# Kernel tuning notes

Hardware: AMD Instinct MI355X
Metric: run time of the kernel (lower is better)

The kernel has to match this reference:

```python
import jax, jax.numpy as jnp
import numpy as np
import math

B, S, H, D = 8, 4096, 768, 64  # batch, seq_len, hidden_dim, head_size


def setup_inputs() -> dict:
    key = jax.random.key(0)
    kx, kk, kq, kv, kbk, kbq, kbv = jax.random.split(key, 7)
    s = 1.0 / math.sqrt(H)
    return {
        "x": jax.random.normal(kx, (B, S, H), dtype=jnp.float32),
        "Wk": jax.random.normal(kk, (H, D), dtype=jnp.float32) * s,
        "bk": jax.random.normal(kbk, (D,), dtype=jnp.float32) * s,
        "Wq": jax.random.normal(kq, (H, D), dtype=jnp.float32) * s,
        "bq": jax.random.normal(kbq, (D,), dtype=jnp.float32) * s,
        "Wv": jax.random.normal(kv, (H, D), dtype=jnp.float32) * s,
        "bv": jax.random.normal(kbv, (D,), dtype=jnp.float32) * s,
    }


def reference(x, Wk, bk, Wq, bq, Wv, bv):
    # projections: [B, S, D]
    k = x @ Wk + bk
    q = x @ Wq + bq
    v = x @ Wv + bv
    # full O(S^2) attention scores, as in the original module
    weight = jnp.einsum("bqd,bkd->bqk", q, k)  # [B, S, S]
    causal = jnp.tril(jnp.ones((S, S), dtype=bool))
    # original masks first, then divides by sqrt(head_size); -inf/sqrt = -inf
    weight = jnp.where(causal, weight, -jnp.inf) / math.sqrt(D)
    weight = jax.nn.softmax(weight, axis=-1)
    # dropout p=0.0 (eval-mode reference): identity
    out = jnp.einsum("bqk,bkd->bqd", weight, v)  # [B, S, D]
    return out
```

## Files before the change

kernel.cpp:

```cpp
#include <hip/hip_runtime.h>
#include <hip/hip_bf16.h>
#include <math.h>

#define B_ 8
#define S_ 4096
#define H_ 768
#define D_ 64

typedef __bf16 bf16;
typedef bf16 bf16x8 __attribute__((ext_vector_type(8)));
typedef bf16 bf16x4 __attribute__((ext_vector_type(4)));
typedef float floatx4 __attribute__((ext_vector_type(4)));
typedef int  int4v  __attribute__((ext_vector_type(4)));

__device__ __forceinline__ int sw_off(int r, int chunk) {
    return r * 128 + ((chunk ^ (r & 7)) << 4);
}

__global__ __launch_bounds__(256) void wtrans_kernel(
    const float* __restrict__ Wq, const float* __restrict__ Wk,
    const float* __restrict__ Wv, bf16* __restrict__ wt)
{
    __shared__ bf16 t_lds[64][72];
    const float* W = (blockIdx.y == 0) ? Wq : (blockIdx.y == 1) ? Wk : Wv;
    bf16* o = wt + ((size_t)blockIdx.y * 12 + blockIdx.x) * 4096;
    const int k0 = blockIdx.x * 64;
    const int tid = threadIdx.x;
    #pragma unroll
    for (int rep = 0; rep < 16; ++rep) {
        int idx = rep * 256 + tid;
        int r = idx >> 6, n = idx & 63;
        t_lds[n][r] = (bf16)W[(size_t)(k0 + r) * D_ + n];
    }
    __syncthreads();
    #pragma unroll
    for (int rep = 0; rep < 16; ++rep) {
        int idx = rep * 256 + tid;
        int n = idx >> 6, kk = idx & 63;
        o[n * 64 + kk] = t_lds[n][kk];
    }
}

__global__ __launch_bounds__(256, 3) void proj_kernel(
    const float* __restrict__ x, const bf16* __restrict__ wt,
    const float* __restrict__ bq, const float* __restrict__ bk,
    const float* __restrict__ bv,
    bf16* __restrict__ qout, bf16* __restrict__ kout, bf16* __restrict__ vtt)
{
    __shared__ bf16 wlds[3][64 * 64];

    const int m0   = blockIdx.x * 64;
    const int tid  = threadIdx.x;
    const int lane = tid & 63;
    const int wave = tid >> 6;
    const int quad = lane >> 4;
    const int c    = lane & 15;
    const int mrow = m0 + wave * 16 + c;

    floatx4 acc[3][4] = {};
    const float* xrow = &x[(size_t)mrow * H_ + quad * 8];

    auto loadA = [&](int k0, bf16x8* dst) {
        #pragma unroll
        for (int s = 0; s < 2; ++s) {
            const float* xp = xrow + k0 + s * 32;
            float4 f0 = *(const float4*)xp;
            float4 f1 = *(const float4*)(xp + 4);
            bf16x8 a;
            a[0] = (bf16)f0.x; a[1] = (bf16)f0.y; a[2] = (bf16)f0.z; a[3] = (bf16)f0.w;
            a[4] = (bf16)f1.x; a[5] = (bf16)f1.y; a[6] = (bf16)f1.z; a[7] = (bf16)f1.w;
            dst[s] = a;
        }
    };
    auto loadW = [&](int kt, int4v g[3][2]) {
        #pragma unroll
        for (int w = 0; w < 3; ++w) {
            const char* s = (const char*)wt + (size_t)(w * 12 + kt) * 8192;
            g[w][0] = *(const int4v*)(s + tid * 16);
            g[w][1] = *(const int4v*)(s + tid * 16 + 4096);
        }
    };

    const int woff = sw_off(tid >> 3, tid & 7);

    bf16x8 afn[2]; loadA(0, afn);
    int4v g[3][2]; loadW(0, g);

    for (int kt = 0; kt < 12; ++kt) {
        __syncthreads();
        #pragma unroll
        for (int w = 0; w < 3; ++w) {
            *(int4v*)((char*)&wlds[w][0] + woff)        = g[w][0];
            *(int4v*)((char*)&wlds[w][0] + woff + 4096) = g[w][1];
        }
        bf16x8 af[2] = { afn[0], afn[1] };
        if (kt < 11) { loadW(kt + 1, g); loadA((kt + 1) * 64, afn); }
        __syncthreads();
        #pragma unroll
        for (int s = 0; s < 2; ++s) {
            #pragma unroll
            for (int w = 0; w < 3; ++w) {
                #pragma unroll
                for (int tn = 0; tn < 4; ++tn) {
                    const int r = tn * 16 + c;
                    bf16x8 bfrag = *(const bf16x8*)
                        ((const char*)&wlds[w][0] + sw_off(r, s * 4 + quad));
                    acc[w][tn] = __builtin_amdgcn_mfma_f32_16x16x32_bf16(
                        af[s], bfrag, acc[w][tn], 0, 0, 0);
                }
            }
        }
    }

    const int rbase = m0 + wave * 16 + quad * 4;
    #pragma unroll
    for (int tn = 0; tn < 4; ++tn) {
        const int n = tn * 16 + c;
        float bqv = bq[n];
        #pragma unroll
        for (int r = 0; r < 4; ++r)
            qout[(size_t)(rbase + r) * 128 + n] = (bf16)(acc[0][tn][r] + bqv);
        float bkv = bk[n];
        #pragma unroll
        for (int r = 0; r < 4; ++r)
            kout[(size_t)(rbase + r) * D_ + n] = (bf16)(acc[1][tn][r] + bkv);
        float bvv = bv[n];
        bf16x4 pk;
        #pragma unroll
        for (int r = 0; r < 4; ++r) pk[r] = (bf16)(acc[2][tn][r] + bvv);
        const int bb = m0 >> 12;
        const int jt = (m0 & 4095) >> 6;
        const int sl = wave * 16 + quad * 4;
        *(bf16x4*)&vtt[(((size_t)bb * 64 + jt) * 64 + n) * 64 + sl] = pk;
    }
}

__global__ __launch_bounds__(256, 3) void attn_kernel(
    const bf16* __restrict__ q, const bf16* __restrict__ k,
    const bf16* __restrict__ vt, float* __restrict__ out)
{
    __shared__ bf16 klds[64 * 64];
    __shared__ bf16 vlds[64 * 64];
    __shared__ bf16 plds[4][16 * 72];

    const int tid  = threadIdx.x;
    const int lane = tid & 63;
    const int wave = tid >> 6;
    const int quad = lane >> 4;
    const int c    = lane & 15;
    const int i    = blockIdx.x;
    const int b    = i & 7;
    const int t    = (i < 256) ? (63 - (i >> 3)) : ((i - 256) >> 3);
    const float cl = 0.18033688011112042f;
    const float M2 = 16.0f;

    const char* ktile0 = (const char*)(k  + (size_t)b * S_ * D_);
    const char* vtile0 = (const char*)(vt + (size_t)b * 64 * 4096);
    bf16* pl = &plds[wave][0];

    bf16x8 qf[2];
    #pragma unroll
    for (int s = 0; s < 2; ++s)
        qf[s] = *(const bf16x8*)
            &q[(size_t)(b * S_ + t * 64 + wave * 16 + c) * 128 + s * 32 + quad * 8];

    floatx4 acc_o[4] = {};
    float lpart[4] = {0.f, 0.f, 0.f, 0.f};

    const int woff = sw_off(tid >> 3, tid & 7);

    int4v gk0, gk1, gv0, gv1;
    gk0 = *(const int4v*)(ktile0 + tid * 16);
    gk1 = *(const int4v*)(ktile0 + tid * 16 + 4096);
    gv0 = *(const int4v*)(vtile0 + tid * 16);
    gv1 = *(const int4v*)(vtile0 + tid * 16 + 4096);

    #pragma unroll 1
    for (int j = 0; j <= t; ++j) {
        __syncthreads();
        *(int4v*)((char*)klds + woff)        = gk0;
        *(int4v*)((char*)klds + woff + 4096) = gk1;
        *(int4v*)((char*)vlds + woff)        = gv0;
        *(int4v*)((char*)vlds + woff + 4096) = gv1;
        if (j < t) {
            const char* ks = ktile0 + (size_t)(j + 1) * 8192;
            const char* vs = vtile0 + (size_t)(j + 1) * 8192;
            gk0 = *(const int4v*)(ks + tid * 16);
            gk1 = *(const int4v*)(ks + tid * 16 + 4096);
            gv0 = *(const int4v*)(vs + tid * 16);
            gv1 = *(const int4v*)(vs + tid * 16 + 4096);
        }
        __syncthreads();

        floatx4 sa[4] = {};
        #pragma unroll
        for (int s = 0; s < 2; ++s)
            #pragma unroll
            for (int tn = 0; tn < 4; ++tn) {
                const int r = tn * 16 + c;
                bf16x8 kf = *(const bf16x8*)
                    ((const char*)klds + sw_off(r, s * 4 + quad));
                sa[tn] = __builtin_amdgcn_mfma_f32_16x16x32_bf16(qf[s], kf, sa[tn], 0, 0, 0);
            }

        if (j == t) {
            #pragma unroll
            for (int tn = 0; tn < 4; ++tn) {
                const int col = tn * 16 + c;
                #pragma unroll
                for (int r = 0; r < 4; ++r)
                    if (col > wave * 16 + quad * 4 + r) sa[tn][r] = -INFINITY;
            }
        }

        #pragma unroll
        for (int tn = 0; tn < 4; ++tn)
            #pragma unroll
            for (int r = 0; r < 4; ++r) {
                float p = __builtin_amdgcn_exp2f(fmaf(sa[tn][r], cl, -M2));
                sa[tn][r] = p;
                lpart[r] += p;
            }

        bf16x8 vf[2][4];
        #pragma unroll
        for (int s = 0; s < 2; ++s)
            #pragma unroll
            for (int tn = 0; tn < 4; ++tn) {
                const int r = tn * 16 + c;
                vf[s][tn] = *(const bf16x8*)
                    ((const char*)vlds + sw_off(r, s * 4 + quad));
            }

        #pragma unroll
        for (int tn = 0; tn < 4; ++tn)
            #pragma unroll
            for (int r = 0; r < 4; ++r)
                pl[(quad * 4 + r) * 72 + tn * 16 + c] = (bf16)sa[tn][r];

        bf16x8 pf[2];
        #pragma unroll
        for (int s = 0; s < 2; ++s)
            pf[s] = *(const bf16x8*)&pl[c * 72 + s * 32 + quad * 8];

        #pragma unroll
        for (int s = 0; s < 2; ++s)
            #pragma unroll
            for (int tn = 0; tn < 4; ++tn)
                acc_o[tn] = __builtin_amdgcn_mfma_f32_16x16x32_bf16(pf[s], vf[s][tn], acc_o[tn], 0, 0, 0);
    }

    #pragma unroll
    for (int r = 0; r < 4; ++r) {
        lpart[r] += __shfl_xor(lpart[r], 1);
        lpart[r] += __shfl_xor(lpart[r], 2);
        lpart[r] += __shfl_xor(lpart[r], 4);
        lpart[r] += __shfl_xor(lpart[r], 8);
    }

    float rl[4];
    #pragma unroll
    for (int r = 0; r < 4; ++r) rl[r] = 1.0f / lpart[r];
    #pragma unroll
    for (int tn = 0; tn < 4; ++tn)
        #pragma unroll
        for (int r = 0; r < 4; ++r)
            out[(size_t)(b * S_ + t * 64 + wave * 16 + quad * 4 + r) * D_ + tn * 16 + c]
                = acc_o[tn][r] * rl[r];
}

extern "C" void kernel_launch(void* const* d_in, const int* in_sizes, int n_in,
                              void* d_out, int out_size, void* d_ws, size_t ws_size,
                              hipStream_t stream) {
    const float* x  = (const float*)d_in[0];
    const float* Wk = (const float*)d_in[1];
    const float* bk = (const float*)d_in[2];
    const float* Wq = (const float*)d_in[3];
    const float* bq = (const float*)d_in[4];
    const float* Wv = (const float*)d_in[5];
    const float* bv = (const float*)d_in[6];
    float* out = (float*)d_out;

    bf16* q_ws  = (bf16*)d_out;
    bf16* k_ws  = (bf16*)d_ws;
    bf16* vt_ws = k_ws + (size_t)B_ * S_ * D_;
    bf16* wt_ws = vt_ws + (size_t)B_ * S_ * D_;

    wtrans_kernel<<<dim3(H_ / 64, 3), 256, 0, stream>>>(Wq, Wk, Wv, wt_ws);
    proj_kernel<<<dim3(B_ * S_ / 64), 256, 0, stream>>>(
        x, wt_ws, bq, bk, bv, q_ws, k_ws, vt_ws);
    attn_kernel<<<dim3(512), 256, 0, stream>>>(q_ws, k_ws, vt_ws, out);
}
```

Before: 218.4 us.

## Halve block sizes: 2-wave projection with 2 row groups, 32-row attention tiles

The projection kernel now uses 128 threads (2 waves), each wave computing 32 rows via two 16-row groups that share every W fragment read from LDS. W tiles are loaded directly each iteration instead of being register-prefetched. The attention kernel switches to 32-query-row blocks (1024 blocks of 2 waves), with the causal mask and loop bound adjusted for half-tile query offsets. This finer work split aims to improve load balance across CUs and reuse of W fragments, at the cost of more K/V tile loads per query row in attention and no W prefetch in projection.

```diff
diff --git a/kernel.cpp b/kernel.cpp
--- a/kernel.cpp
+++ b/kernel.cpp
@@ -41,7 +41,7 @@
     }
 }
 
-__global__ __launch_bounds__(256, 3) void proj_kernel(
+__global__ __launch_bounds__(128, 2) void proj_kernel(
     const float* __restrict__ x, const bf16* __restrict__ wt,
     const float* __restrict__ bq, const float* __restrict__ bk,
     const float* __restrict__ bv,
@@ -55,93 +55,104 @@
     const int wave = tid >> 6;
     const int quad = lane >> 4;
     const int c    = lane & 15;
-    const int mrow = m0 + wave * 16 + c;
-
-    floatx4 acc[3][4] = {};
-    const float* xrow = &x[(size_t)mrow * H_ + quad * 8];
-
-    auto loadA = [&](int k0, bf16x8* dst) {
-        #pragma unroll
-        for (int s = 0; s < 2; ++s) {
-            const float* xp = xrow + k0 + s * 32;
-            float4 f0 = *(const float4*)xp;
-            float4 f1 = *(const float4*)(xp + 4);
-            bf16x8 a;
-            a[0] = (bf16)f0.x; a[1] = (bf16)f0.y; a[2] = (bf16)f0.z; a[3] = (bf16)f0.w;
-            a[4] = (bf16)f1.x; a[5] = (bf16)f1.y; a[6] = (bf16)f1.z; a[7] = (bf16)f1.w;
-            dst[s] = a;
-        }
+
+    floatx4 acc[2][3][4] = {};
+
+    const float* xrow[2];
+    #pragma unroll
+    for (int g = 0; g < 2; ++g)
+        xrow[g] = &x[(size_t)(m0 + wave * 32 + g * 16 + c) * H_ + quad * 8];
+
+    auto loadA = [&](int k0, bf16x8 dst[2][2]) {
+        #pragma unroll
+        for (int g = 0; g < 2; ++g)
+            #pragma unroll
+            for (int s = 0; s < 2; ++s) {
+                const float* xp = xrow[g] + k0 + s * 32;
+                float4 f0 = *(const float4*)xp;
+                float4 f1 = *(const float4*)(xp + 4);
+                bf16x8 a;
+                a[0] = (bf16)f0.x; a[1] = (bf16)f0.y; a[2] = (bf16)f0.z; a[3] = (bf16)f0.w;
+                a[4] = (bf16)f1.x; a[5] = (bf16)f1.y; a[6] = (bf16)f1.z; a[7] = (bf16)f1.w;
+                dst[g][s] = a;
+            }
     };
-    auto loadW = [&](int kt, int4v g[3][2]) {
-        #pragma unroll
-        for (int w = 0; w < 3; ++w) {
-            const char* s = (const char*)wt + (size_t)(w * 12 + kt) * 8192;
-            g[w][0] = *(const int4v*)(s + tid * 16);
-            g[w][1] = *(const int4v*)(s + tid * 16 + 4096);
-        }
-    };
-
-    const int woff = sw_off(tid >> 3, tid & 7);
-
-    bf16x8 afn[2]; loadA(0, afn);
-    int4v g[3][2]; loadW(0, g);
+
+    int loff[4];
+    #pragma unroll
+    for (int n = 0; n < 4; ++n) {
+        int off = tid * 16 + n * 2048;
+        loff[n] = sw_off(off >> 7, (off >> 4) & 7);
+    }
+
+    bf16x8 afn[2][2]; loadA(0, afn);
 
     for (int kt = 0; kt < 12; ++kt) {
         __syncthreads();
         #pragma unroll
         for (int w = 0; w < 3; ++w) {
-            *(int4v*)((char*)&wlds[w][0] + woff)        = g[w][0];
-            *(int4v*)((char*)&wlds[w][0] + woff + 4096) = g[w][1];
-        }
-        bf16x8 af[2] = { afn[0], afn[1] };
-        if (kt < 11) { loadW(kt + 1, g); loadA((kt + 1) * 64, afn); }
+            const char* src = (const char*)wt + (size_t)(w * 12 + kt) * 8192;
+            int4v tmp[4];
+            #pragma unroll
+            for (int n = 0; n < 4; ++n)
+                tmp[n] = *(const int4v*)(src + tid * 16 + n * 2048);
+            #pragma unroll
+            for (int n = 0; n < 4; ++n)
+                *(int4v*)((char*)&wlds[w][0] + loff[n]) = tmp[n];
+        }
+        bf16x8 af[2][2];
+        #pragma unroll
+        for (int g = 0; g < 2; ++g) { af[g][0] = afn[g][0]; af[g][1] = afn[g][1]; }
+        if (kt < 11) loadA((kt + 1) * 64, afn);
         __syncthreads();
         #pragma unroll
-        for (int s = 0; s < 2; ++s) {
-            #pragma unroll
-            for (int w = 0; w < 3; ++w) {
+        for (int s = 0; s < 2; ++s)
+            #pragma unroll
+            for (int w = 0; w < 3; ++w)
                 #pragma unroll
                 for (int tn = 0; tn < 4; ++tn) {
-                    const int r = tn * 16 + c;
                     bf16x8 bfrag = *(const bf16x8*)
-                        ((const char*)&wlds[w][0] + sw_off(r, s * 4 + quad));
-                    acc[w][tn] = __builtin_amdgcn_mfma_f32_16x16x32_bf16(
-                        af[s], bfrag, acc[w][tn], 0, 0, 0);
+                        ((const char*)&wlds[w][0] + sw_off(tn * 16 + c, s * 4 + quad));
+                    #pragma unroll
+                    for (int g = 0; g < 2; ++g)
+                        acc[g][w][tn] = __builtin_amdgcn_mfma_f32_16x16x32_bf16(
+                            af[g][s], bfrag, acc[g][w][tn], 0, 0, 0);
                 }
-            }
-        }
-    }
-
-    const int rbase = m0 + wave * 16 + quad * 4;
-    #pragma unroll
-    for (int tn = 0; tn < 4; ++tn) {
-        const int n = tn * 16 + c;
-        float bqv = bq[n];
-        #pragma unroll
-        for (int r = 0; r < 4; ++r)
-            qout[(size_t)(rbase + r) * 128 + n] = (bf16)(acc[0][tn][r] + bqv);
-        float bkv = bk[n];
-        #pragma unroll
-        for (int r = 0; r < 4; ++r)
-            kout[(size_t)(rbase + r) * D_ + n] = (bf16)(acc[1][tn][r] + bkv);
-        float bvv = bv[n];
-        bf16x4 pk;
-        #pragma unroll
-        for (int r = 0; r < 4; ++r) pk[r] = (bf16)(acc[2][tn][r] + bvv);
-        const int bb = m0 >> 12;
-        const int jt = (m0 & 4095) >> 6;
-        const int sl = wave * 16 + quad * 4;
-        *(bf16x4*)&vtt[(((size_t)bb * 64 + jt) * 64 + n) * 64 + sl] = pk;
-    }
-}
-
-__global__ __launch_bounds__(256, 3) void attn_kernel(
+    }
+
+    #pragma unroll
+    for (int g = 0; g < 2; ++g) {
+        const int rbase = m0 + wave * 32 + g * 16 + quad * 4;
+        #pragma unroll
+        for (int tn = 0; tn < 4; ++tn) {
+            const int n = tn * 16 + c;
+            float bqv = bq[n];
+            #pragma unroll
+            for (int r = 0; r < 4; ++r)
+                qout[(size_t)(rbase + r) * 128 + n] = (bf16)(acc[g][0][tn][r] + bqv);
+            float bkv = bk[n];
+            #pragma unroll
+            for (int r = 0; r < 4; ++r)
+                kout[(size_t)(rbase + r) * D_ + n] = (bf16)(acc[g][1][tn][r] + bkv);
+            float bvv = bv[n];
+            bf16x4 pk;
+            #pragma unroll
+            for (int r = 0; r < 4; ++r) pk[r] = (bf16)(acc[g][2][tn][r] + bvv);
+            const int bb = m0 >> 12;
+            const int jt = (m0 & 4095) >> 6;
+            const int sl = wave * 32 + g * 16 + quad * 4;
+            *(bf16x4*)&vtt[(((size_t)bb * 64 + jt) * 64 + n) * 64 + sl] = pk;
+        }
+    }
+}
+
+__global__ __launch_bounds__(128, 2) void attn_kernel(
     const bf16* __restrict__ q, const bf16* __restrict__ k,
     const bf16* __restrict__ vt, float* __restrict__ out)
 {
     __shared__ bf16 klds[64 * 64];
     __shared__ bf16 vlds[64 * 64];
-    __shared__ bf16 plds[4][16 * 72];
+    __shared__ bf16 plds[2][16 * 72];
 
     const int tid  = threadIdx.x;
     const int lane = tid & 63;
@@ -150,7 +161,8 @@
     const int c    = lane & 15;
     const int i    = blockIdx.x;
     const int b    = i & 7;
-    const int t    = (i < 256) ? (63 - (i >> 3)) : ((i - 256) >> 3);
+    const int t    = (i < 512) ? (127 - (i >> 3)) : ((i - 512) >> 3);
+    const int jmax = t >> 1;
     const float cl = 0.18033688011112042f;
     const float M2 = 16.0f;
 
@@ -158,37 +170,45 @@
     const char* vtile0 = (const char*)(vt + (size_t)b * 64 * 4096);
     bf16* pl = &plds[wave][0];
 
+    int loff[4];
+    #pragma unroll
+    for (int n = 0; n < 4; ++n) {
+        int off = tid * 16 + n * 2048;
+        loff[n] = sw_off(off >> 7, (off >> 4) & 7);
+    }
+
     bf16x8 qf[2];
     #pragma unroll
     for (int s = 0; s < 2; ++s)
         qf[s] = *(const bf16x8*)
-            &q[(size_t)(b * S_ + t * 64 + wave * 16 + c) * 128 + s * 32 + quad * 8];
+            &q[(size_t)(b * S_ + t * 32 + wave * 16 + c) * 128 + s * 32 + quad * 8];
 
     floatx4 acc_o[4] = {};
     float lpart[4] = {0.f, 0.f, 0.f, 0.f};
 
-    const int woff = sw_off(tid >> 3, tid & 7);
-
-    int4v gk0, gk1, gv0, gv1;
-    gk0 = *(const int4v*)(ktile0 + tid * 16);
-    gk1 = *(const int4v*)(ktile0 + tid * 16 + 4096);
-    gv0 = *(const int4v*)(vtile0 + tid * 16);
-    gv1 = *(const int4v*)(vtile0 + tid * 16 + 4096);
+    int4v gk[4], gv[4];
+    #pragma unroll
+    for (int n = 0; n < 4; ++n) {
+        gk[n] = *(const int4v*)(ktile0 + tid * 16 + n * 2048);
+        gv[n] = *(const int4v*)(vtile0 + tid * 16 + n * 2048);
+    }
 
     #pragma unroll 1
-    for (int j = 0; j <= t; ++j) {
+    for (int j = 0; j <= jmax; ++j) {
         __syncthreads();
-        *(int4v*)((char*)klds + woff)        = gk0;
-        *(int4v*)((char*)klds + woff + 4096) = gk1;
-        *(int4v*)((char*)vlds + woff)        = gv0;
-        *(int4v*)((char*)vlds + woff + 4096) = gv1;
-        if (j < t) {
+        #pragma unroll
+        for (int n = 0; n < 4; ++n) {
+            *(int4v*)((char*)klds + loff[n]) = gk[n];
+            *(int4v*)((char*)vlds + loff[n]) = gv[n];
+        }
+        if (j < jmax) {
             const char* ks = ktile0 + (size_t)(j + 1) * 8192;
             const char* vs = vtile0 + (size_t)(j + 1) * 8192;
-            gk0 = *(const int4v*)(ks + tid * 16);
-            gk1 = *(const int4v*)(ks + tid * 16 + 4096);
-            gv0 = *(const int4v*)(vs + tid * 16);
-            gv1 = *(const int4v*)(vs + tid * 16 + 4096);
+            #pragma unroll
+            for (int n = 0; n < 4; ++n) {
+                gk[n] = *(const int4v*)(ks + tid * 16 + n * 2048);
+                gv[n] = *(const int4v*)(vs + tid * 16 + n * 2048);
+            }
         }
         __syncthreads();
 
@@ -197,19 +217,18 @@
         for (int s = 0; s < 2; ++s)
             #pragma unroll
             for (int tn = 0; tn < 4; ++tn) {
-                const int r = tn * 16 + c;
                 bf16x8 kf = *(const bf16x8*)
-                    ((const char*)klds + sw_off(r, s * 4 + quad));
+                    ((const char*)klds + sw_off(tn * 16 + c, s * 4 + quad));
                 sa[tn] = __builtin_amdgcn_mfma_f32_16x16x32_bf16(qf[s], kf, sa[tn], 0, 0, 0);
             }
 
-        if (j == t) {
+        if (j == jmax) {
             #pragma unroll
             for (int tn = 0; tn < 4; ++tn) {
-                const int col = tn * 16 + c;
+                const int col = j * 64 + tn * 16 + c;
                 #pragma unroll
                 for (int r = 0; r < 4; ++r)
-                    if (col > wave * 16 + quad * 4 + r) sa[tn][r] = -INFINITY;
+                    if (col > t * 32 + wave * 16 + quad * 4 + r) sa[tn][r] = -INFINITY;
             }
         }
 
@@ -226,11 +245,9 @@
         #pragma unroll
         for (int s = 0; s < 2; ++s)
             #pragma unroll
-            for (int tn = 0; tn < 4; ++tn) {
-                const int r = tn * 16 + c;
+            for (int tn = 0; tn < 4; ++tn)
                 vf[s][tn] = *(const bf16x8*)
-                    ((const char*)vlds + sw_off(r, s * 4 + quad));
-            }
+                    ((const char*)vlds + sw_off(tn * 16 + c, s * 4 + quad));
 
         #pragma unroll
         for (int tn = 0; tn < 4; ++tn)
@@ -265,7 +282,7 @@
     for (int tn = 0; tn < 4; ++tn)
         #pragma unroll
         for (int r = 0; r < 4; ++r)
-            out[(size_t)(b * S_ + t * 64 + wave * 16 + quad * 4 + r) * D_ + tn * 16 + c]
+            out[(size_t)(b * S_ + t * 32 + wave * 16 + quad * 4 + r) * D_ + tn * 16 + c]
                 = acc_o[tn][r] * rl[r];
 }
 
@@ -287,7 +304,7 @@
     bf16* wt_ws = vt_ws + (size_t)B_ * S_ * D_;
 
     wtrans_kernel<<<dim3(H_ / 64, 3), 256, 0, stream>>>(Wq, Wk, Wv, wt_ws);
-    proj_kernel<<<dim3(B_ * S_ / 64), 256, 0, stream>>>(
+    proj_kernel<<<dim3(B_ * S_ / 64), 128, 0, stream>>>(
         x, wt_ws, bq, bk, bv, q_ws, k_ws, vt_ws);
-    attn_kernel<<<dim3(512), 256, 0, stream>>>(q_ws, k_ws, vt_ws, out);
-}
+    attn_kernel<<<dim3(1024), 128, 0, stream>>>(q_ws, k_ws, vt_ws, out);
+}
```

Result: slower. 253.4 us (+16.0%).

## Stage K/V and weight tiles via direct global-to-LDS DMA with double buffering

Applied to the files above, without the earlier changes.

Replaces the register-staged global loads and LDS stores in the projection and attention kernels with 16-byte global_load_lds transfers into double-buffered LDS tiles. This drops one barrier per loop iteration. The swizzle now lives in the global layout: the weight-transpose and projection kernels write K, V^T and W in pre-swizzled 64x64 tiles. The aim is to cut VGPR pressure and the extra LDS store traffic, and to overlap the next tile's load with the current tile's compute. In exchange, LDS use doubles and the launch-bounds occupancy hint drops from 3 to 2 blocks, and correctness relies on the barrier waiting for the outstanding DMA.

```diff
diff --git a/kernel.cpp b/kernel.cpp
--- a/kernel.cpp
+++ b/kernel.cpp
@@ -11,10 +11,19 @@
 typedef bf16 bf16x8 __attribute__((ext_vector_type(8)));
 typedef bf16 bf16x4 __attribute__((ext_vector_type(4)));
 typedef float floatx4 __attribute__((ext_vector_type(4)));
-typedef int  int4v  __attribute__((ext_vector_type(4)));
 
 __device__ __forceinline__ int sw_off(int r, int chunk) {
     return r * 128 + ((chunk ^ (r & 7)) << 4);
+}
+__device__ __forceinline__ int sw_elem(int r, int e) {
+    return r * 64 + (((e >> 3) ^ (r & 7)) << 3) + (e & 7);
+}
+
+__device__ __forceinline__ void dma16(const bf16* gsrc, bf16* ldst) {
+    __builtin_amdgcn_global_load_lds(
+        (const __attribute__((address_space(1))) unsigned int*)(const void*)gsrc,
+        (__attribute__((address_space(3))) unsigned int*)(void*)ldst,
+        16, 0, 0);
 }
 
 __global__ __launch_bounds__(256) void wtrans_kernel(
@@ -37,17 +46,17 @@
     for (int rep = 0; rep < 16; ++rep) {
         int idx = rep * 256 + tid;
         int n = idx >> 6, kk = idx & 63;
-        o[n * 64 + kk] = t_lds[n][kk];
-    }
-}
-
-__global__ __launch_bounds__(256, 3) void proj_kernel(
+        o[sw_elem(n, kk)] = t_lds[n][kk];
+    }
+}
+
+__global__ __launch_bounds__(256, 2) void proj_kernel(
     const float* __restrict__ x, const bf16* __restrict__ wt,
     const float* __restrict__ bq, const float* __restrict__ bk,
     const float* __restrict__ bv,
     bf16* __restrict__ qout, bf16* __restrict__ kout, bf16* __restrict__ vtt)
 {
-    __shared__ bf16 wlds[3][64 * 64];
+    __shared__ bf16 wlds[2][3][4096];
 
     const int m0   = blockIdx.x * 64;
     const int tid  = threadIdx.x;
@@ -72,47 +81,42 @@
             dst[s] = a;
         }
     };
-    auto loadW = [&](int kt, int4v g[3][2]) {
+    auto stageW = [&](int kt, int buf) {
         #pragma unroll
         for (int w = 0; w < 3; ++w) {
-            const char* s = (const char*)wt + (size_t)(w * 12 + kt) * 8192;
-            g[w][0] = *(const int4v*)(s + tid * 16);
-            g[w][1] = *(const int4v*)(s + tid * 16 + 4096);
+            const bf16* src = wt + (size_t)(w * 12 + kt) * 4096 + wave * 1024 + lane * 8;
+            bf16* dst = &wlds[buf][w][wave * 1024];
+            dma16(src, dst);
+            dma16(src + 512, dst + 512);
         }
     };
 
-    const int woff = sw_off(tid >> 3, tid & 7);
-
     bf16x8 afn[2]; loadA(0, afn);
-    int4v g[3][2]; loadW(0, g);
+    stageW(0, 0);
 
     for (int kt = 0; kt < 12; ++kt) {
         __syncthreads();
-        #pragma unroll
-        for (int w = 0; w < 3; ++w) {
-            *(int4v*)((char*)&wlds[w][0] + woff)        = g[w][0];
-            *(int4v*)((char*)&wlds[w][0] + woff + 4096) = g[w][1];
-        }
+        const int cur = kt & 1;
+        if (kt < 11) stageW(kt + 1, 1 - cur);
         bf16x8 af[2] = { afn[0], afn[1] };
-        if (kt < 11) { loadW(kt + 1, g); loadA((kt + 1) * 64, afn); }
-        __syncthreads();
-        #pragma unroll
-        for (int s = 0; s < 2; ++s) {
-            #pragma unroll
-            for (int w = 0; w < 3; ++w) {
+        if (kt < 11) loadA((kt + 1) * 64, afn);
+        #pragma unroll
+        for (int s = 0; s < 2; ++s)
+            #pragma unroll
+            for (int w = 0; w < 3; ++w)
                 #pragma unroll
                 for (int tn = 0; tn < 4; ++tn) {
-                    const int r = tn * 16 + c;
                     bf16x8 bfrag = *(const bf16x8*)
-                        ((const char*)&wlds[w][0] + sw_off(r, s * 4 + quad));
+                        ((const char*)&wlds[cur][w][0] + sw_off(tn * 16 + c, s * 4 + quad));
                     acc[w][tn] = __builtin_amdgcn_mfma_f32_16x16x32_bf16(
                         af[s], bfrag, acc[w][tn], 0, 0, 0);
                 }
-            }
-        }
     }
 
     const int rbase = m0 + wave * 16 + quad * 4;
+    const int bb = m0 >> 12;
+    const int jt = (m0 & 4095) >> 6;
+    const size_t tbase = ((size_t)bb * 64 + jt) * 4096;
     #pragma unroll
     for (int tn = 0; tn < 4; ++tn) {
         const int n = tn * 16 + c;
@@ -122,25 +126,25 @@
             qout[(size_t)(rbase + r) * 128 + n] = (bf16)(acc[0][tn][r] + bqv);
         float bkv = bk[n];
         #pragma unroll
-        for (int r = 0; r < 4; ++r)
-            kout[(size_t)(rbase + r) * D_ + n] = (bf16)(acc[1][tn][r] + bkv);
+        for (int r = 0; r < 4; ++r) {
+            const int sl = (rbase & 63) + r;
+            kout[tbase + sw_elem(sl, n)] = (bf16)(acc[1][tn][r] + bkv);
+        }
         float bvv = bv[n];
         bf16x4 pk;
         #pragma unroll
         for (int r = 0; r < 4; ++r) pk[r] = (bf16)(acc[2][tn][r] + bvv);
-        const int bb = m0 >> 12;
-        const int jt = (m0 & 4095) >> 6;
-        const int sl = wave * 16 + quad * 4;
-        *(bf16x4*)&vtt[(((size_t)bb * 64 + jt) * 64 + n) * 64 + sl] = pk;
-    }
-}
-
-__global__ __launch_bounds__(256, 3) void attn_kernel(
+        const int sl0 = (rbase & 63);
+        *(bf16x4*)&vtt[tbase + sw_elem(n, sl0)] = pk;
+    }
+}
+
+__global__ __launch_bounds__(256, 2) void attn_kernel(
     const bf16* __restrict__ q, const bf16* __restrict__ k,
     const bf16* __restrict__ vt, float* __restrict__ out)
 {
-    __shared__ bf16 klds[64 * 64];
-    __shared__ bf16 vlds[64 * 64];
+    __shared__ bf16 klds[2][4096];
+    __shared__ bf16 vlds[2][4096];
     __shared__ bf16 plds[4][16 * 72];
 
     const int tid  = threadIdx.x;
@@ -154,9 +158,16 @@
     const float cl = 0.18033688011112042f;
     const float M2 = 16.0f;
 
-    const char* ktile0 = (const char*)(k  + (size_t)b * S_ * D_);
-    const char* vtile0 = (const char*)(vt + (size_t)b * 64 * 4096);
+    const bf16* ktile0 = k  + (size_t)b * 64 * 4096;
+    const bf16* vtile0 = vt + (size_t)b * 64 * 4096;
     bf16* pl = &plds[wave][0];
+
+    auto stage = [&](const bf16* gsrc, bf16* ldst) {
+        const bf16* s = gsrc + wave * 1024 + lane * 8;
+        bf16* d = ldst + wave * 1024;
+        dma16(s, d);
+        dma16(s + 512, d + 512);
+    };
 
     bf16x8 qf[2];
     #pragma unroll
@@ -167,39 +178,25 @@
     floatx4 acc_o[4] = {};
     float lpart[4] = {0.f, 0.f, 0.f, 0.f};
 
-    const int woff = sw_off(tid >> 3, tid & 7);
-
-    int4v gk0, gk1, gv0, gv1;
-    gk0 = *(const int4v*)(ktile0 + tid * 16);
-    gk1 = *(const int4v*)(ktile0 + tid * 16 + 4096);
-    gv0 = *(const int4v*)(vtile0 + tid * 16);
-    gv1 = *(const int4v*)(vtile0 + tid * 16 + 4096);
+    stage(ktile0, klds[0]);
+    stage(vtile0, vlds[0]);
 
     #pragma unroll 1
     for (int j = 0; j <= t; ++j) {
         __syncthreads();
-        *(int4v*)((char*)klds + woff)        = gk0;
-        *(int4v*)((char*)klds + woff + 4096) = gk1;
-        *(int4v*)((char*)vlds + woff)        = gv0;
-        *(int4v*)((char*)vlds + woff + 4096) = gv1;
+        const int cur = j & 1;
         if (j < t) {
-            const char* ks = ktile0 + (size_t)(j + 1) * 8192;
-            const char* vs = vtile0 + (size_t)(j + 1) * 8192;
-            gk0 = *(const int4v*)(ks + tid * 16);
-            gk1 = *(const int4v*)(ks + tid * 16 + 4096);
-            gv0 = *(const int4v*)(vs + tid * 16);
-            gv1 = *(const int4v*)(vs + tid * 16 + 4096);
-        }
-        __syncthreads();
+            stage(ktile0 + (size_t)(j + 1) * 4096, klds[1 - cur]);
+            stage(vtile0 + (size_t)(j + 1) * 4096, vlds[1 - cur]);
+        }
 
         floatx4 sa[4] = {};
         #pragma unroll
         for (int s = 0; s < 2; ++s)
             #pragma unroll
             for (int tn = 0; tn < 4; ++tn) {
-                const int r = tn * 16 + c;
                 bf16x8 kf = *(const bf16x8*)
-                    ((const char*)klds + sw_off(r, s * 4 + quad));
+                    ((const char*)&klds[cur][0] + sw_off(tn * 16 + c, s * 4 + quad));
                 sa[tn] = __builtin_amdgcn_mfma_f32_16x16x32_bf16(qf[s], kf, sa[tn], 0, 0, 0);
             }
 
@@ -226,11 +223,9 @@
         #pragma unroll
         for (int s = 0; s < 2; ++s)
             #pragma unroll
-            for (int tn = 0; tn < 4; ++tn) {
-                const int r = tn * 16 + c;
+            for (int tn = 0; tn < 4; ++tn)
                 vf[s][tn] = *(const bf16x8*)
-                    ((const char*)vlds + sw_off(r, s * 4 + quad));
-            }
+                    ((const char*)&vlds[cur][0] + sw_off(tn * 16 + c, s * 4 + quad));
 
         #pragma unroll
         for (int tn = 0; tn < 4; ++tn)
```

Measured after the change: 232.8 us. 6.6% more time.
